# Optimization experiments

Hardware: AMD Instinct MI355X
Metric: run time of the kernel (lower is better)

The kernel has to match this reference:

```python
import jax, jax.numpy as jnp
import numpy as np

N_NODES = 100000
N_EDGES = 1600000
NF = 64
EF = 32
BN_EPS = 1e-5


def setup_inputs() -> dict:
    key = jax.random.key(0)
    ks = jax.random.split(key, 12)
    node_feats = jax.random.normal(ks[0], (N_NODES, NF), dtype=jnp.float32)
    edge_feats = jax.random.normal(ks[1], (N_EDGES, EF), dtype=jnp.float32)
    src = jax.random.randint(ks[2], (N_EDGES,), 0, N_NODES, dtype=jnp.int32)
    dst = jax.random.randint(ks[3], (N_EDGES,), 0, N_NODES, dtype=jnp.int32)
    # Linear params stored as [in, out]; scaled like torch default init (1/sqrt(in)).
    def lin(k, fin, fout):
        k1, k2 = jax.random.split(k)
        bound = 1.0 / np.sqrt(fin)
        W = jax.random.uniform(k1, (fin, fout), jnp.float32, -bound, bound)
        b = jax.random.uniform(k2, (fout,), jnp.float32, -bound, bound)
        return W, b
    W_src, b_src = lin(ks[4], NF, 2 * NF)
    W_dst, b_dst = lin(ks[5], NF, 2 * NF)
    W_edge, b_edge = lin(ks[6], EF, 2 * NF)
    gamma_m = jnp.ones((2 * NF,), jnp.float32)
    beta_m = jnp.zeros((2 * NF,), jnp.float32)
    gamma_n = jnp.ones((NF,), jnp.float32)
    beta_n = jnp.zeros((NF,), jnp.float32)
    return {
        "node_feats": node_feats, "edge_feats": edge_feats,
        "W_src": W_src, "b_src": b_src,
        "W_dst": W_dst, "b_dst": b_dst,
        "W_edge": W_edge, "b_edge": b_edge,
        "gamma_m": gamma_m, "beta_m": beta_m,
        "gamma_n": gamma_n, "beta_n": beta_n,
        "src": src, "dst": dst,
    }


def _batchnorm(x, gamma, beta):
    # Training-mode batch norm with biased variance (as torch BatchNorm1d in train).
    mean = jnp.mean(x, axis=0)
    var = jnp.var(x, axis=0)
    return (x - mean) * (gamma * jax.lax.rsqrt(var + BN_EPS)) + beta


def reference(node_feats, edge_feats, W_src, b_src, W_dst, b_dst, W_edge, b_edge,
              gamma_m, beta_m, gamma_n, beta_n, src, dst):
    h_src = node_feats @ W_src + b_src            # [N, 2F]
    h_dst = node_feats @ W_dst + b_dst            # [N, 2F]
    # u_add_v edge gather + edge linear
    m = h_src[src] + h_dst[dst] + (edge_feats @ W_edge + b_edge)  # [E, 2F]
    m = _batchnorm(m, gamma_m, beta_m)
    h_f, h_s = m[:, :NF], m[:, NF:]
    m = jax.nn.sigmoid(h_f) * jax.nn.softplus(h_s)  # gated message [E, F]
    # scatter-sum messages to destination nodes
    h = jax.ops.segment_sum(m, dst, num_segments=N_NODES)  # [N, F]
    h = _batchnorm(h, gamma_n, beta_n)
    return jax.nn.softplus(node_feats + h)
```

## Files before the change

### kernel.cpp

```cpp
#include <hip/hip_runtime.h>
#include <hip/hip_bf16.h>
#include <stdint.h>

#define NNODES 100000
#define NEDGES 1600000
#define C2 128
#define EFEAT 32
#define BN_EPS 1e-5f
#define SCAN_B ((NNODES + 255) / 256)

typedef __hip_bfloat16 bf16;

__device__ __forceinline__ float bflo(uint32_t u) { return __uint_as_float(u << 16); }
__device__ __forceinline__ float bfhi(uint32_t u) { return __uint_as_float(u & 0xffff0000u); }
__device__ __forceinline__ float sigm(float x) { return 1.0f / (1.0f + __expf(-x)); }
__device__ __forceinline__ float softp(float x) { return fmaxf(x, 0.0f) + __logf(1.0f + __expf(-fabsf(x))); }
__device__ __forceinline__ uint32_t pk2(float a, float b) {
    union { bf16 h[2]; uint32_t u; } pk;
    pk.h[0] = __float2bfloat16(a);
    pk.h[1] = __float2bfloat16(b);
    return pk.u;
}

struct TB {};
struct TF {};

template <class T> struct LD;
template <> struct LD<TB> {
    static __device__ __forceinline__ float ld(const void* p, size_t i) {
        return __bfloat162float(((const bf16*)p)[i]);
    }
    static __device__ __forceinline__ float2 ld2(const void* p, size_t i) {
        const uint32_t u = *(const uint32_t*)((const bf16*)p + i);
        return make_float2(bflo(u), bfhi(u));
    }
    static __device__ __forceinline__ void st2(void* p, size_t i, float a, float b) {
        *(uint32_t*)((bf16*)p + i) = pk2(a, b);
    }
    static __device__ __forceinline__ void ldrow(const void* p, size_t e, uint4* o) {
        const uint4* er = (const uint4*)p + e * 4;
        o[0] = er[0]; o[1] = er[1]; o[2] = er[2]; o[3] = er[3];
    }
};
template <> struct LD<TF> {
    static __device__ __forceinline__ float ld(const void* p, size_t i) {
        return ((const float*)p)[i];
    }
    static __device__ __forceinline__ float2 ld2(const void* p, size_t i) {
        return *(const float2*)((const float*)p + i);
    }
    static __device__ __forceinline__ void st2(void* p, size_t i, float a, float b) {
        *(float2*)((float*)p + i) = make_float2(a, b);
    }
    static __device__ __forceinline__ void ldrow(const void* p, size_t e, uint4* o) {
        const float4* fr = (const float4*)p + e * 8;
#pragma unroll
        for (int j = 0; j < 4; ++j) {
            const float4 a = fr[2 * j], b = fr[2 * j + 1];
            o[j] = make_uint4(pk2(a.x, a.y), pk2(a.z, a.w), pk2(b.x, b.y), pk2(b.z, b.w));
        }
    }
};

__global__ void k_detect(const uint32_t* __restrict__ nodeb, int* __restrict__ flag) {
    __shared__ int sfp;
    if (threadIdx.x == 0) sfp = 0;
    __syncthreads();
    const float v = fabsf(bflo(nodeb[threadIdx.x]));
    if (v > 1e10f) sfp = 1;
    __syncthreads();
    if (threadIdx.x == 0) *flag = sfp;
}

__global__ __launch_bounds__(256) void k_hist(const int* __restrict__ dst,
                                              int* __restrict__ cnt) {
    for (int e = blockIdx.x * 256 + threadIdx.x; e < NEDGES; e += gridDim.x * 256)
        atomicAdd(&cnt[dst[e]], 1);
}

__global__ __launch_bounds__(256) void k_scan1(const int* __restrict__ cnt,
                                               int* __restrict__ bsum) {
    __shared__ int red[256];
    const int t = threadIdx.x;
    const int i = blockIdx.x * 256 + t;
    red[t] = (i < NNODES) ? cnt[i] : 0;
    __syncthreads();
    for (int s = 128; s > 0; s >>= 1) {
        if (t < s) red[t] += red[t + s];
        __syncthreads();
    }
    if (t == 0) bsum[blockIdx.x] = red[0];
}

__global__ void k_scan2(int* __restrict__ bsum) {
    __shared__ int sh[512];
    const int t = threadIdx.x;
    const int v0 = (t < SCAN_B) ? bsum[t] : 0;
    sh[t] = v0;
    __syncthreads();
    for (int ofs = 1; ofs < 512; ofs <<= 1) {
        const int v = (t >= ofs) ? sh[t - ofs] : 0;
        __syncthreads();
        sh[t] += v;
        __syncthreads();
    }
    if (t < SCAN_B) bsum[t] = sh[t] - v0;
}

__global__ __launch_bounds__(256) void k_scan3(const int* __restrict__ cnt,
                                               const int* __restrict__ bsum,
                                               int* __restrict__ off,
                                               int* __restrict__ cur) {
    __shared__ int sh[256];
    const int t = threadIdx.x;
    const int i = blockIdx.x * 256 + t;
    const int orig = (i < NNODES) ? cnt[i] : 0;
    sh[t] = orig;
    __syncthreads();
    for (int ofs = 1; ofs < 256; ofs <<= 1) {
        const int v = (t >= ofs) ? sh[t - ofs] : 0;
        __syncthreads();
        sh[t] += v;
        __syncthreads();
    }
    const int excl = sh[t] - orig + bsum[blockIdx.x];
    if (i < NNODES) { off[i] = excl; cur[i] = excl; }
    if (i == NNODES) off[NNODES] = excl;
}

template <class T>
__device__ __forceinline__ void fill_body(const int* __restrict__ dst,
                                          const int* __restrict__ src,
                                          const void* __restrict__ ef,
                                          int* __restrict__ cur,
                                          int* __restrict__ srcp,
                                          uint4* __restrict__ efp4)
{
    for (int e = blockIdx.x * 256 + threadIdx.x; e < NEDGES; e += gridDim.x * 256) {
        uint4 o[4];
        LD<T>::ldrow(ef, e, o);
        const int p = atomicAdd(&cur[dst[e]], 1);
        srcp[p] = src[e];
        uint4* w = efp4 + (size_t)p * 4;
        w[0] = o[0]; w[1] = o[1]; w[2] = o[2]; w[3] = o[3];
    }
}

__global__ __launch_bounds__(256) void k_fill(const int* __restrict__ dst,
                                              const int* __restrict__ src,
                                              const void* __restrict__ ef,
                                              int* __restrict__ cur,
                                              int* __restrict__ srcp,
                                              uint4* __restrict__ efp4,
                                              const int* __restrict__ flag)
{
    if (*flag) fill_body<TF>(dst, src, ef, cur, srcp, efp4);
    else       fill_body<TB>(dst, src, ef, cur, srcp, efp4);
}

template <class T>
__device__ __forceinline__ void tables_body(
    const void* node, const void* Wsrc, const void* bsrc,
    const void* Wdst, const void* bdst, bf16* tsrc, bf16* tdst, float* x)
{
    const int t = threadIdx.x;
    const int col = t & 127;
    const void* W = (t < 128) ? Wsrc : Wdst;
    float w[64];
#pragma unroll
    for (int k = 0; k < 64; ++k) w[k] = LD<T>::ld(W, k * C2 + col);
    const float b = (t < 128) ? LD<T>::ld(bsrc, col) : LD<T>::ld(bdst, col);
    bf16* tab = (t < 128) ? tsrc : tdst;
    const int pos = (col < 64) ? (2 * col) : (2 * col - 127);
    for (int base = blockIdx.x * 4; base < NNODES; base += gridDim.x * 4) {
        x[t] = LD<T>::ld(node, (size_t)base * 64 + t);
        __syncthreads();
        float a0 = b, a1 = b, a2 = b, a3 = b;
#pragma unroll
        for (int k = 0; k < 64; ++k) {
            const float wv = w[k];
            a0 = fmaf(x[k], wv, a0);
            a1 = fmaf(x[64 + k], wv, a1);
            a2 = fmaf(x[128 + k], wv, a2);
            a3 = fmaf(x[192 + k], wv, a3);
        }
        __syncthreads();
        tab[(size_t)(base + 0) * C2 + pos] = __float2bfloat16(a0);
        tab[(size_t)(base + 1) * C2 + pos] = __float2bfloat16(a1);
        tab[(size_t)(base + 2) * C2 + pos] = __float2bfloat16(a2);
        tab[(size_t)(base + 3) * C2 + pos] = __float2bfloat16(a3);
    }
}

__global__ __launch_bounds__(256, 4) void k_tables(
    const void* node, const void* Wsrc, const void* bsrc,
    const void* Wdst, const void* bdst, bf16* tsrc, bf16* tdst, const int* flag)
{
    __shared__ float x[256];
    if (*flag) tables_body<TF>(node, Wsrc, bsrc, Wdst, bdst, tsrc, tdst, x);
    else       tables_body<TB>(node, Wsrc, bsrc, Wdst, bdst, tsrc, tdst, x);
}

template <class T>
__device__ __forceinline__ void fin_m_body(const float* mstats, const void* gamma,
                                           const void* beta, float* mss)
{
    const int c = threadIdx.x;
    const float inv = 1.0f / (float)NEDGES;
    const float mean = mstats[c] * inv;
    const float var = fmaxf(mstats[C2 + c] * inv - mean * mean, 0.0f);
    const float sc = LD<T>::ld(gamma, c) * rsqrtf(var + BN_EPS);
    mss[c] = sc;
    mss[C2 + c] = LD<T>::ld(beta, c) - mean * sc;
}

__global__ void k_fin_m(const float* mstats, const void* gamma, const void* beta,
                        float* mss, const int* flag)
{
    if (*flag) fin_m_body<TF>(mstats, gamma, beta, mss);
    else       fin_m_body<TB>(mstats, gamma, beta, mss);
}

#define EFMAD(ua, ub, W0v, W1v) {                                   \
    const float fx = bflo(ua), fy = bfhi(ua);                       \
    const float fz = bflo(ub), fw = bfhi(ub);                       \
    el0 = fmaf(fx, (W0v).x, el0); el1 = fmaf(fx, (W1v).x, el1);     \
    el0 = fmaf(fy, (W0v).y, el0); el1 = fmaf(fy, (W1v).y, el1);     \
    el0 = fmaf(fz, (W0v).z, el0); el1 = fmaf(fz, (W1v).z, el1);     \
    el0 = fmaf(fw, (W0v).w, el0); el1 = fmaf(fw, (W1v).w, el1); }

#define LDW(j)                                                                       \
    const float4 W0##j = make_float4(LD<T>::ld(We, (4 * j + 0) * C2 + c),            \
                                     LD<T>::ld(We, (4 * j + 1) * C2 + c),            \
                                     LD<T>::ld(We, (4 * j + 2) * C2 + c),            \
                                     LD<T>::ld(We, (4 * j + 3) * C2 + c));           \
    const float4 W1##j = make_float4(LD<T>::ld(We, (4 * j + 0) * C2 + c + 64),       \
                                     LD<T>::ld(We, (4 * j + 1) * C2 + c + 64),       \
                                     LD<T>::ld(We, (4 * j + 2) * C2 + c + 64),       \
                                     LD<T>::ld(We, (4 * j + 3) * C2 + c + 64));

template <class T, bool STATS>
__device__ __forceinline__ void edge_pass_body(
    const uint4* __restrict__ efp4, const int* __restrict__ srcp,
    const void* __restrict__ We, const void* __restrict__ be,
    const uint32_t* __restrict__ tsrc, const uint32_t* __restrict__ tdst,
    const float* __restrict__ mss, const int* __restrict__ off,
    float* __restrict__ hacc, float* __restrict__ ost, float* __restrict__ red)
{
    const int t = threadIdx.x;
    const int c = t & 63;
    const int g = t >> 6;
    LDW(0) LDW(1) LDW(2) LDW(3) LDW(4) LDW(5) LDW(6) LDW(7)
    const float be0 = LD<T>::ld(be, c), be1 = LD<T>::ld(be, c + 64);
    float sc0 = 0.f, sh0 = 0.f, sc1 = 0.f, sh1 = 0.f;
    if constexpr (!STATS) {
        sc0 = mss[c];      sh0 = mss[C2 + c];
        sc1 = mss[c + 64]; sh1 = mss[C2 + c + 64];
    }
    float s0 = 0.f, q0 = 0.f, s1 = 0.f, q1 = 0.f;
    for (int d0 = blockIdx.x * 4; d0 < NNODES; d0 += gridDim.x * 4) {
        const int d = d0 + g;
        const uint32_t ud = tdst[(size_t)d * 64 + c];
        const float hd0 = bflo(ud), hd1 = bfhi(ud);
        const int beg = __builtin_amdgcn_readfirstlane(off[d]);
        const int end = __builtin_amdgcn_readfirstlane(off[d + 1]);
        float acc = 0.f;
        for (int b = beg; b < end; b += 64) {
            const int nb = min(64, end - b);
            const int sb = (b + c < end) ? srcp[b + c] : 0;
            uint4 n0, n1, n2, n3;
            {
                const uint4* rp = efp4 + (size_t)b * 4;
                n0 = rp[0]; n1 = rp[1]; n2 = rp[2]; n3 = rp[3];
            }
            uint32_t usn = tsrc[(size_t)__shfl(sb, 0, 64) * 64 + c];
            for (int i = 0; i < nb; ++i) {
                const uint4 r0 = n0, r1 = n1, r2 = n2, r3 = n3;
                const uint32_t us = usn;
                if (i + 1 < nb) {
                    const uint4* rp = efp4 + (size_t)(b + i + 1) * 4;
                    n0 = rp[0]; n1 = rp[1]; n2 = rp[2]; n3 = rp[3];
                    usn = tsrc[(size_t)__shfl(sb, i + 1, 64) * 64 + c];
                }
                float el0 = be0, el1 = be1;
                EFMAD(r0.x, r0.y, W00, W10) EFMAD(r0.z, r0.w, W01, W11)
                EFMAD(r1.x, r1.y, W02, W12) EFMAD(r1.z, r1.w, W03, W13)
                EFMAD(r2.x, r2.y, W04, W14) EFMAD(r2.z, r2.w, W05, W15)
                EFMAD(r3.x, r3.y, W06, W16) EFMAD(r3.z, r3.w, W07, W17)
                const float m0 = el0 + bflo(us) + hd0;
                const float m1 = el1 + bfhi(us) + hd1;
                if constexpr (STATS) {
                    s0 += m0; q0 += m0 * m0;
                    s1 += m1; q1 += m1 * m1;
                } else {
                    acc += sigm(fmaf(m0, sc0, sh0)) * softp(fmaf(m1, sc1, sh1));
                }
            }
        }
        if constexpr (!STATS) {
            hacc[(size_t)d * 64 + c] = acc;
            s0 += acc; q0 += acc * acc;
        }
    }
    if constexpr (STATS) {
        ((float4*)red)[t] = make_float4(s0, q0, s1, q1);
        __syncthreads();
        if (t < 64) {
            float a0 = 0.f, a1 = 0.f, a2 = 0.f, a3 = 0.f;
            for (int gg = 0; gg < 4; ++gg) {
                const float4 r = ((const float4*)red)[gg * 64 + t];
                a0 += r.x; a1 += r.y; a2 += r.z; a3 += r.w;
            }
            atomicAdd(&ost[t], a0);
            atomicAdd(&ost[C2 + t], a1);
            atomicAdd(&ost[t + 64], a2);
            atomicAdd(&ost[C2 + t + 64], a3);
        }
    } else {
        red[t] = s0; red[256 + t] = q0;
        __syncthreads();
        if (t < 64) {
            float a = 0.f, b2 = 0.f;
            for (int gg = 0; gg < 4; ++gg) {
                a += red[gg * 64 + t];
                b2 += red[256 + gg * 64 + t];
            }
            atomicAdd(&ost[t], a);
            atomicAdd(&ost[64 + t], b2);
        }
    }
}

template <bool STATS>
__global__ __attribute__((amdgpu_waves_per_eu(4, 4))) __launch_bounds__(256)
void k_edge_pass(
    const uint4* __restrict__ efp4, const int* __restrict__ srcp,
    const void* __restrict__ We, const void* __restrict__ be,
    const uint32_t* __restrict__ tsrc, const uint32_t* __restrict__ tdst,
    const float* __restrict__ mss, const int* __restrict__ off,
    float* __restrict__ hacc, float* __restrict__ ost, const int* __restrict__ flag)
{
    __shared__ float red[1024];
    if (*flag) edge_pass_body<TF, STATS>(efp4, srcp, We, be, tsrc, tdst, mss, off, hacc, ost, red);
    else       edge_pass_body<TB, STATS>(efp4, srcp, We, be, tsrc, tdst, mss, off, hacc, ost, red);
}

template <class T>
__device__ __forceinline__ void fin_n_body(const float* nstats, const void* gamma,
                                           const void* beta, float* nss)
{
    const int c = threadIdx.x;
    const float inv = 1.0f / (float)NNODES;
    const float mean = nstats[c] * inv;
    const float var = fmaxf(nstats[64 + c] * inv - mean * mean, 0.0f);
    const float sc = LD<T>::ld(gamma, c) * rsqrtf(var + BN_EPS);
    nss[c] = sc;
    nss[64 + c] = LD<T>::ld(beta, c) - mean * sc;
}

__global__ void k_fin_n(const float* nstats, const void* gamma, const void* beta,
                        float* nss, const int* flag)
{
    if (*flag) fin_n_body<TF>(nstats, gamma, beta, nss);
    else       fin_n_body<TB>(nstats, gamma, beta, nss);
}

template <class T>
__device__ __forceinline__ void out_body(const void* node, const float* hacc,
                                         const float* nss, void* out)
{
    const int t = threadIdx.x;
    const int64_t npairs = (int64_t)NNODES * 32;
    int64_t i = (int64_t)blockIdx.x * 256 + t;
    const int c0 = (int)((i * 2) & 63);
    const float sc0 = nss[c0], sh0 = nss[64 + c0];
    const float sc1 = nss[c0 + 1], sh1 = nss[64 + c0 + 1];
    const float2* hp = (const float2*)hacc;
    const int64_t stride = (int64_t)gridDim.x * 256;
    for (; i < npairs; i += stride) {
        const float2 nv = LD<T>::ld2(node, (size_t)(2 * i));
        const float2 h = hp[i];
        const float v0 = softp(nv.x + fmaf(h.x, sc0, sh0));
        const float v1 = softp(nv.y + fmaf(h.y, sc1, sh1));
        LD<T>::st2(out, (size_t)(2 * i), v0, v1);
    }
}

__global__ __launch_bounds__(256) void k_out(const void* node, const float* hacc,
                                             const float* nss, void* out, const int* flag)
{
    if (*flag) out_body<TF>(node, hacc, nss, out);
    else       out_body<TB>(node, hacc, nss, out);
}

extern "C" void kernel_launch(void* const* d_in, const int* in_sizes, int n_in,
                              void* d_out, int out_size, void* d_ws, size_t ws_size,
                              hipStream_t stream)
{
    const void* node = d_in[0];
    const void* ef   = d_in[1];
    const void* Wsrc = d_in[2];
    const void* bsrc = d_in[3];
    const void* Wdst = d_in[4];
    const void* bdst = d_in[5];
    const void* We   = d_in[6];
    const void* be   = d_in[7];
    const void* gm   = d_in[8];
    const void* bm   = d_in[9];
    const void* gn   = d_in[10];
    const void* bn   = d_in[11];
    const int* src   = (const int*)d_in[12];
    const int* dst   = (const int*)d_in[13];

    float* hacc   = (float*)d_ws;
    float* mstats = hacc + (size_t)NNODES * 64;
    float* nstats = mstats + 256;
    float* mss    = nstats + 128;
    float* nss    = mss + 256;
    int* flag     = (int*)(nss + 128);
    bf16* tsrc    = (bf16*)(flag + 4);
    bf16* tdst    = tsrc + (size_t)NNODES * C2;
    int* cnt      = (int*)(tdst + (size_t)NNODES * C2);
    int* off      = cnt + NNODES;
    int* cur      = off + NNODES + 1;
    int* bsum     = cur + NNODES;
    int* srcp     = bsum + 512;
    bf16* efp     = (bf16*)((((uintptr_t)(srcp + NEDGES)) + 15) & ~(uintptr_t)15);

    hipMemsetAsync(mstats, 0, 384 * sizeof(float), stream);
    hipMemsetAsync(cnt, 0, NNODES * sizeof(int), stream);
    k_detect<<<1, 256, 0, stream>>>((const uint32_t*)node, flag);
    k_hist<<<2048, 256, 0, stream>>>(dst, cnt);
    k_scan1<<<SCAN_B, 256, 0, stream>>>(cnt, bsum);
    k_scan2<<<1, 512, 0, stream>>>(bsum);
    k_scan3<<<SCAN_B, 256, 0, stream>>>(cnt, bsum, off, cur);
    k_fill<<<2048, 256, 0, stream>>>(dst, src, ef, cur, srcp, (uint4*)efp, flag);
    k_tables<<<512, 256, 0, stream>>>(node, Wsrc, bsrc, Wdst, bdst, tsrc, tdst, flag);
    k_edge_pass<true><<<2048, 256, 0, stream>>>(
        (const uint4*)efp, srcp, We, be,
        (const uint32_t*)tsrc, (const uint32_t*)tdst,
        mss, off, hacc, mstats, flag);
    k_fin_m<<<1, 128, 0, stream>>>(mstats, gm, bm, mss, flag);
    k_edge_pass<false><<<2048, 256, 0, stream>>>(
        (const uint4*)efp, srcp, We, be,
        (const uint32_t*)tsrc, (const uint32_t*)tdst,
        mss, off, hacc, nstats, flag);
    k_fin_n<<<1, 64, 0, stream>>>(nstats, gn, bn, nss, flag);
    k_out<<<1024, 256, 0, stream>>>(node, hacc, nss, d_out, flag);
}
```

Before: 1.209 ms.

## Compute edge linear with bf16 MFMA tiles of 16 edges per wave

Replaces the per-lane scalar FMA edge-feature projection in both edge passes with 16x16x32 bf16 MFMA instructions, processing 16 CSR edges per step and producing all 128 output channels from 8 MFMAs. A new one-block kernel prepacks W_edge into the MFMA B-operand layout. Per-channel stats and message reductions are restructured around the MFMA output layout using cross-lane shuffles, and launch bounds change from fixed waves-per-EU to 3 blocks. This trades ALU work for matrix-core use, but wastes lanes for nodes whose degree is not a multiple of 16, and the gathered source-table rows are now fetched per edge per row group.

```diff
diff --git a/kernel.cpp b/kernel.cpp
--- a/kernel.cpp
+++ b/kernel.cpp
@@ -10,6 +10,10 @@
 #define SCAN_B ((NNODES + 255) / 256)
 
 typedef __hip_bfloat16 bf16;
+typedef __attribute__((ext_vector_type(8))) short bf16x8;
+typedef __attribute__((ext_vector_type(4))) float f32x4;
+
+union U8 { uint4 u; bf16x8 h; };
 
 __device__ __forceinline__ float bflo(uint32_t u) { return __uint_as_float(u << 16); }
 __device__ __forceinline__ float bfhi(uint32_t u) { return __uint_as_float(u & 0xffff0000u); }
@@ -21,6 +25,9 @@
     pk.h[1] = __float2bfloat16(b);
     return pk.u;
 }
+__device__ __forceinline__ f32x4 mfma16(bf16x8 a, bf16x8 b, f32x4 c) {
+    return __builtin_amdgcn_mfma_f32_16x16x32_bf16(a, b, c, 0, 0, 0);
+}
 
 struct TB {};
 struct TF {};
@@ -159,6 +166,28 @@
 }
 
 template <class T>
+__device__ __forceinline__ void prepw_body(const void* __restrict__ We,
+                                           uint4* __restrict__ Wep4)
+{
+    const int t = threadIdx.x;
+    const int n = t >> 6, l = t & 63;
+    const int col = l & 15, kg = l >> 4;
+    float w[8];
+#pragma unroll
+    for (int j = 0; j < 8; ++j)
+        w[j] = LD<T>::ld(We, (size_t)(kg * 8 + j) * C2 + n * 16 + col);
+    Wep4[n * 64 + l] = make_uint4(pk2(w[0], w[1]), pk2(w[2], w[3]),
+                                  pk2(w[4], w[5]), pk2(w[6], w[7]));
+}
+
+__global__ void k_prepw(const void* __restrict__ We, uint4* __restrict__ Wep4,
+                        const int* __restrict__ flag)
+{
+    if (*flag) prepw_body<TF>(We, Wep4);
+    else       prepw_body<TB>(We, Wep4);
+}
+
+template <class T>
 __device__ __forceinline__ void tables_body(
     const void* node, const void* Wsrc, const void* bsrc,
     const void* Wdst, const void* bdst, bf16* tsrc, bf16* tdst, float* x)
@@ -221,128 +250,152 @@
     else       fin_m_body<TB>(mstats, gamma, beta, mss);
 }
 
-#define EFMAD(ua, ub, W0v, W1v) {                                   \
-    const float fx = bflo(ua), fy = bfhi(ua);                       \
-    const float fz = bflo(ub), fw = bfhi(ub);                       \
-    el0 = fmaf(fx, (W0v).x, el0); el1 = fmaf(fx, (W1v).x, el1);     \
-    el0 = fmaf(fy, (W0v).y, el0); el1 = fmaf(fy, (W1v).y, el1);     \
-    el0 = fmaf(fz, (W0v).z, el0); el1 = fmaf(fz, (W1v).z, el1);     \
-    el0 = fmaf(fw, (W0v).w, el0); el1 = fmaf(fw, (W1v).w, el1); }
-
-#define LDW(j)                                                                       \
-    const float4 W0##j = make_float4(LD<T>::ld(We, (4 * j + 0) * C2 + c),            \
-                                     LD<T>::ld(We, (4 * j + 1) * C2 + c),            \
-                                     LD<T>::ld(We, (4 * j + 2) * C2 + c),            \
-                                     LD<T>::ld(We, (4 * j + 3) * C2 + c));           \
-    const float4 W1##j = make_float4(LD<T>::ld(We, (4 * j + 0) * C2 + c + 64),       \
-                                     LD<T>::ld(We, (4 * j + 1) * C2 + c + 64),       \
-                                     LD<T>::ld(We, (4 * j + 2) * C2 + c + 64),       \
-                                     LD<T>::ld(We, (4 * j + 3) * C2 + c + 64));
-
 template <class T, bool STATS>
 __device__ __forceinline__ void edge_pass_body(
     const uint4* __restrict__ efp4, const int* __restrict__ srcp,
-    const void* __restrict__ We, const void* __restrict__ be,
-    const uint32_t* __restrict__ tsrc, const uint32_t* __restrict__ tdst,
+    const uint4* __restrict__ Wep4, const void* __restrict__ be,
+    const uint32_t* __restrict__ ts32, const uint32_t* __restrict__ td32,
     const float* __restrict__ mss, const int* __restrict__ off,
     float* __restrict__ hacc, float* __restrict__ ost, float* __restrict__ red)
 {
     const int t = threadIdx.x;
-    const int c = t & 63;
-    const int g = t >> 6;
-    LDW(0) LDW(1) LDW(2) LDW(3) LDW(4) LDW(5) LDW(6) LDW(7)
-    const float be0 = LD<T>::ld(be, c), be1 = LD<T>::ld(be, c + 64);
-    float sc0 = 0.f, sh0 = 0.f, sc1 = 0.f, sh1 = 0.f;
-    if constexpr (!STATS) {
-        sc0 = mss[c];      sh0 = mss[C2 + c];
-        sc1 = mss[c + 64]; sh1 = mss[C2 + c + 64];
-    }
-    float s0 = 0.f, q0 = 0.f, s1 = 0.f, q1 = 0.f;
+    const int lane = t & 63, wv = t >> 6;
+    const int r16 = lane & 15, kg = lane >> 4;
+    U8 b[8];
+#pragma unroll
+    for (int n = 0; n < 8; ++n) b[n].u = Wep4[n * 64 + lane];
+    float beL[4], beH[4], scL[4], shL[4], scH[4], shH[4];
+#pragma unroll
+    for (int n = 0; n < 4; ++n) {
+        const int ch = n * 16 + r16;
+        beL[n] = LD<T>::ld(be, ch);
+        beH[n] = LD<T>::ld(be, ch + 64);
+        if constexpr (!STATS) {
+            scL[n] = mss[ch];       shL[n] = mss[C2 + ch];
+            scH[n] = mss[ch + 64];  shH[n] = mss[C2 + ch + 64];
+        }
+    }
+    float sL[4] = {0,0,0,0}, qL[4] = {0,0,0,0};
+    float sH[4] = {0,0,0,0}, qH[4] = {0,0,0,0};
+    float ns[4] = {0,0,0,0}, nq[4] = {0,0,0,0};
+    const f32x4 zero = {0.f, 0.f, 0.f, 0.f};
     for (int d0 = blockIdx.x * 4; d0 < NNODES; d0 += gridDim.x * 4) {
-        const int d = d0 + g;
-        const uint32_t ud = tdst[(size_t)d * 64 + c];
-        const float hd0 = bflo(ud), hd1 = bfhi(ud);
+        const int d = d0 + wv;
         const int beg = __builtin_amdgcn_readfirstlane(off[d]);
         const int end = __builtin_amdgcn_readfirstlane(off[d + 1]);
-        float acc = 0.f;
-        for (int b = beg; b < end; b += 64) {
-            const int nb = min(64, end - b);
-            const int sb = (b + c < end) ? srcp[b + c] : 0;
-            uint4 n0, n1, n2, n3;
-            {
-                const uint4* rp = efp4 + (size_t)b * 4;
-                n0 = rp[0]; n1 = rp[1]; n2 = rp[2]; n3 = rp[3];
-            }
-            uint32_t usn = tsrc[(size_t)__shfl(sb, 0, 64) * 64 + c];
-            for (int i = 0; i < nb; ++i) {
-                const uint4 r0 = n0, r1 = n1, r2 = n2, r3 = n3;
-                const uint32_t us = usn;
-                if (i + 1 < nb) {
-                    const uint4* rp = efp4 + (size_t)(b + i + 1) * 4;
-                    n0 = rp[0]; n1 = rp[1]; n2 = rp[2]; n3 = rp[3];
-                    usn = tsrc[(size_t)__shfl(sb, i + 1, 64) * 64 + c];
-                }
-                float el0 = be0, el1 = be1;
-                EFMAD(r0.x, r0.y, W00, W10) EFMAD(r0.z, r0.w, W01, W11)
-                EFMAD(r1.x, r1.y, W02, W12) EFMAD(r1.z, r1.w, W03, W13)
-                EFMAD(r2.x, r2.y, W04, W14) EFMAD(r2.z, r2.w, W05, W15)
-                EFMAD(r3.x, r3.y, W06, W16) EFMAD(r3.z, r3.w, W07, W17)
-                const float m0 = el0 + bflo(us) + hd0;
-                const float m1 = el1 + bfhi(us) + hd1;
-                if constexpr (STATS) {
-                    s0 += m0; q0 += m0 * m0;
-                    s1 += m1; q1 += m1 * m1;
-                } else {
-                    acc += sigm(fmaf(m0, sc0, sh0)) * softp(fmaf(m1, sc1, sh1));
+        uint32_t ud[4];
+#pragma unroll
+        for (int n = 0; n < 4; ++n) ud[n] = td32[(size_t)d * 64 + n * 16 + r16];
+        float gacc[4] = {0.f, 0.f, 0.f, 0.f};
+        for (int e0 = beg; e0 < end; e0 += 16) {
+            const int arow = min(e0 + r16, NEDGES - 1);
+            U8 a; a.u = efp4[(size_t)arow * 4 + kg];
+            f32x4 acc[8];
+#pragma unroll
+            for (int n = 0; n < 8; ++n) acc[n] = mfma16(a.h, b[n].h, zero);
+#pragma unroll
+            for (int r = 0; r < 4; ++r) {
+                const int e = e0 + kg * 4 + r;
+                const bool valid = (e < end);
+                const int sn = srcp[valid ? e : beg];
+                const uint32_t* bs = ts32 + (size_t)sn * 64;
+#pragma unroll
+                for (int n = 0; n < 4; ++n) {
+                    const uint32_t us = bs[n * 16 + r16];
+                    const float m0 = acc[n][r] + beL[n] + bflo(us) + bflo(ud[n]);
+                    const float m1 = acc[n + 4][r] + beH[n] + bfhi(us) + bfhi(ud[n]);
+                    if constexpr (STATS) {
+                        const float m0v = valid ? m0 : 0.f;
+                        const float m1v = valid ? m1 : 0.f;
+                        sL[n] += m0v; qL[n] += m0v * m0v;
+                        sH[n] += m1v; qH[n] += m1v * m1v;
+                    } else {
+                        const float g = sigm(fmaf(m0, scL[n], shL[n])) *
+                                        softp(fmaf(m1, scH[n], shH[n]));
+                        gacc[n] += valid ? g : 0.f;
+                    }
                 }
             }
         }
         if constexpr (!STATS) {
-            hacc[(size_t)d * 64 + c] = acc;
-            s0 += acc; q0 += acc * acc;
+#pragma unroll
+            for (int n = 0; n < 4; ++n) {
+                gacc[n] += __shfl_xor(gacc[n], 16);
+                gacc[n] += __shfl_xor(gacc[n], 32);
+            }
+            if (lane < 16) {
+#pragma unroll
+                for (int n = 0; n < 4; ++n) {
+                    hacc[(size_t)d * 64 + n * 16 + r16] = gacc[n];
+                    ns[n] += gacc[n];
+                    nq[n] += gacc[n] * gacc[n];
+                }
+            }
         }
     }
     if constexpr (STATS) {
-        ((float4*)red)[t] = make_float4(s0, q0, s1, q1);
-        __syncthreads();
-        if (t < 64) {
-            float a0 = 0.f, a1 = 0.f, a2 = 0.f, a3 = 0.f;
-            for (int gg = 0; gg < 4; ++gg) {
-                const float4 r = ((const float4*)red)[gg * 64 + t];
-                a0 += r.x; a1 += r.y; a2 += r.z; a3 += r.w;
+        float vals[16];
+#pragma unroll
+        for (int n = 0; n < 4; ++n) {
+            vals[n * 4 + 0] = sL[n]; vals[n * 4 + 1] = qL[n];
+            vals[n * 4 + 2] = sH[n]; vals[n * 4 + 3] = qH[n];
+        }
+#pragma unroll
+        for (int v = 0; v < 16; ++v) {
+            vals[v] += __shfl_xor(vals[v], 16);
+            vals[v] += __shfl_xor(vals[v], 32);
+        }
+        if (lane < 16) {
+#pragma unroll
+            for (int v = 0; v < 16; ++v) red[wv * 256 + r16 * 16 + v] = vals[v];
+        }
+        __syncthreads();
+        {
+            const int col = t >> 4, v = t & 15;
+            const int n = v >> 2, part = v & 3;
+            float s = 0.f;
+#pragma unroll
+            for (int w = 0; w < 4; ++w) s += red[w * 256 + col * 16 + v];
+            const int ch = n * 16 + col;
+            int idx;
+            if (part == 0) idx = ch;
+            else if (part == 1) idx = C2 + ch;
+            else if (part == 2) idx = ch + 64;
+            else idx = C2 + ch + 64;
+            atomicAdd(&ost[idx], s);
+        }
+    } else {
+        if (lane < 16) {
+#pragma unroll
+            for (int n = 0; n < 4; ++n) {
+                red[wv * 128 + r16 * 8 + n] = ns[n];
+                red[wv * 128 + r16 * 8 + 4 + n] = nq[n];
             }
-            atomicAdd(&ost[t], a0);
-            atomicAdd(&ost[C2 + t], a1);
-            atomicAdd(&ost[t + 64], a2);
-            atomicAdd(&ost[C2 + t + 64], a3);
-        }
-    } else {
-        red[t] = s0; red[256 + t] = q0;
-        __syncthreads();
-        if (t < 64) {
-            float a = 0.f, b2 = 0.f;
-            for (int gg = 0; gg < 4; ++gg) {
-                a += red[gg * 64 + t];
-                b2 += red[256 + gg * 64 + t];
-            }
-            atomicAdd(&ost[t], a);
-            atomicAdd(&ost[64 + t], b2);
+        }
+        __syncthreads();
+        if (t < 128) {
+            float s = 0.f;
+#pragma unroll
+            for (int w = 0; w < 4; ++w) s += red[w * 128 + t];
+            const int r16d = t >> 3, rest = t & 7;
+            const int n = rest & 3, isq = rest >> 2;
+            const int ch = n * 16 + r16d;
+            atomicAdd(&ost[isq * 64 + ch], s);
         }
     }
 }
 
 template <bool STATS>
-__global__ __attribute__((amdgpu_waves_per_eu(4, 4))) __launch_bounds__(256)
-void k_edge_pass(
+__global__ __launch_bounds__(256, 3) void k_edge_pass(
     const uint4* __restrict__ efp4, const int* __restrict__ srcp,
-    const void* __restrict__ We, const void* __restrict__ be,
-    const uint32_t* __restrict__ tsrc, const uint32_t* __restrict__ tdst,
+    const uint4* __restrict__ Wep4, const void* __restrict__ be,
+    const uint32_t* __restrict__ ts32, const uint32_t* __restrict__ td32,
     const float* __restrict__ mss, const int* __restrict__ off,
     float* __restrict__ hacc, float* __restrict__ ost, const int* __restrict__ flag)
 {
     __shared__ float red[1024];
-    if (*flag) edge_pass_body<TF, STATS>(efp4, srcp, We, be, tsrc, tdst, mss, off, hacc, ost, red);
-    else       edge_pass_body<TB, STATS>(efp4, srcp, We, be, tsrc, tdst, mss, off, hacc, ost, red);
+    if (*flag) edge_pass_body<TF, STATS>(efp4, srcp, Wep4, be, ts32, td32, mss, off, hacc, ost, red);
+    else       edge_pass_body<TB, STATS>(efp4, srcp, Wep4, be, ts32, td32, mss, off, hacc, ost, red);
 }
 
 template <class T>
@@ -426,6 +479,7 @@
     int* bsum     = cur + NNODES;
     int* srcp     = bsum + 512;
     bf16* efp     = (bf16*)((((uintptr_t)(srcp + NEDGES)) + 15) & ~(uintptr_t)15);
+    uint4* Wep4   = (uint4*)(efp + (size_t)NEDGES * EFEAT);
 
     hipMemsetAsync(mstats, 0, 384 * sizeof(float), stream);
     hipMemsetAsync(cnt, 0, NNODES * sizeof(int), stream);
@@ -435,14 +489,15 @@
     k_scan2<<<1, 512, 0, stream>>>(bsum);
     k_scan3<<<SCAN_B, 256, 0, stream>>>(cnt, bsum, off, cur);
     k_fill<<<2048, 256, 0, stream>>>(dst, src, ef, cur, srcp, (uint4*)efp, flag);
+    k_prepw<<<1, 512, 0, stream>>>(We, Wep4, flag);
     k_tables<<<512, 256, 0, stream>>>(node, Wsrc, bsrc, Wdst, bdst, tsrc, tdst, flag);
     k_edge_pass<true><<<2048, 256, 0, stream>>>(
-        (const uint4*)efp, srcp, We, be,
+        (const uint4*)efp, srcp, Wep4, be,
         (const uint32_t*)tsrc, (const uint32_t*)tdst,
         mss, off, hacc, mstats, flag);
     k_fin_m<<<1, 128, 0, stream>>>(mstats, gm, bm, mss, flag);
     k_edge_pass<false><<<2048, 256, 0, stream>>>(
-        (const uint4*)efp, srcp, We, be,
+        (const uint4*)efp, srcp, Wep4, be,
         (const uint32_t*)tsrc, (const uint32_t*)tdst,
         mss, off, hacc, nstats, flag);
     k_fin_n<<<1, 64, 0, stream>>>(nstats, gn, bn, nss, flag);
```

Result: faster. 1.072 ms (-11.3%).
